# Kernel optimization log

Hardware: AMD Instinct MI355X
Metric: run time of the kernel (lower is better)

## Reference

```python
import jax, jax.numpy as jnp
import numpy as np

BATCH, SEQ, FEAT, UNITS, OUT = 128, 2048, 64, 64, 6


def setup_inputs() -> dict:
    key = jax.random.key(0)
    ks = jax.random.split(key, 12)
    s = 0.05
    inp = {
        "x": jax.random.normal(ks[0], (BATCH, SEQ, FEAT), dtype=jnp.float32),
        # LSTMCell 0 (kernel, recurrent_kernel, bias); gate order i,f,g,o
        "W0": jax.random.normal(ks[1], (FEAT, 4 * UNITS), dtype=jnp.float32) * s,
        "U0": jax.random.normal(ks[2], (UNITS, 4 * UNITS), dtype=jnp.float32) * s,
        "b0": jax.random.normal(ks[3], (4 * UNITS,), dtype=jnp.float32) * s,
        # LSTMCell 1 (shared by layers 2 AND 3, as in the original code)
        "W1": jax.random.normal(ks[4], (UNITS, 4 * UNITS), dtype=jnp.float32) * s,
        "U1": jax.random.normal(ks[5], (UNITS, 4 * UNITS), dtype=jnp.float32) * s,
        "b1": jax.random.normal(ks[6], (4 * UNITS,), dtype=jnp.float32) * s,
        # Dense heads
        "Wf": jax.random.normal(ks[7], (UNITS, 64), dtype=jnp.float32) * s,
        "bf": jax.random.normal(ks[8], (64,), dtype=jnp.float32) * s,
        "Wo": jax.random.normal(ks[9], (64, OUT), dtype=jnp.float32) * s,
        "bo": jax.random.normal(ks[10], (OUT,), dtype=jnp.float32) * s,
    }
    return inp


def _lstm_cell(c, h, xin, W, U, b):
    # Keras LSTMCell math, gate order i, f, g(candidate), o
    z = xin @ W + h @ U + b  # [B, 4U]
    i, f, g, o = jnp.split(z, 4, axis=-1)
    c_new = jax.nn.sigmoid(f) * c + jax.nn.sigmoid(i) * jnp.tanh(g)
    h_new = jax.nn.sigmoid(o) * jnp.tanh(c_new)
    return c_new, h_new


def reference(x, W0, U0, b0, W1, U1, b1, Wf, bf, Wo, bo):
    B = x.shape[0]
    z = jnp.zeros((B, UNITS), dtype=x.dtype)
    init = (z, z, z, z, z, z)  # (c0,h0,c1,h1,c2,h2)

    def step(carry, xt):
        c0, h0, c1, h1, c2, h2 = carry
        c0, h0 = _lstm_cell(c0, h0, xt, W0, U0, b0)
        c1, h1 = _lstm_cell(c1, h1, h0, W1, U1, b1)
        # NOTE: original code reuses rnn_cell1's weights for the 3rd layer
        c2, h2 = _lstm_cell(c2, h2, h1, W1, U1, b1)
        return (c0, h0, c1, h1, c2, h2), None

    xt = jnp.swapaxes(x, 0, 1)  # [T, B, F]
    (c0, h0, c1, h1, c2, h2), _ = jax.lax.scan(step, init, xt)
    y = jax.nn.relu(h2 @ Wf + bf)
    return y @ Wo + bo
```

## Files before the change

### kernel.cpp

```cpp
#include <hip/hip_runtime.h>

#define BATCHN 128
#define SEQT   2048
#define FEAT   64
#define UNITS  64
#define NCOL   256
#define OUTD   6
#define CH     20
#define BUF    96

typedef float v2f __attribute__((ext_vector_type(2)));

__device__ __forceinline__ float fast_exp2(float x) {
#if __has_builtin(__builtin_amdgcn_exp2f)
    return __builtin_amdgcn_exp2f(x);
#else
    return exp2f(x);
#endif
}
__device__ __forceinline__ float fast_rcp(float x) {
#if __has_builtin(__builtin_amdgcn_rcpf)
    return __builtin_amdgcn_rcpf(x);
#else
    return 1.0f / x;
#endif
}
__device__ __forceinline__ float sig_(float x) {
    return fast_rcp(1.0f + fast_exp2(-1.4426950408889634f * x));
}
__device__ __forceinline__ float tanh_(float x) {
    float xc = fminf(fmaxf(x, -15.0f), 15.0f);
    float e  = fast_exp2(2.8853900817779268f * xc);
    return (e - 1.0f) * fast_rcp(e + 1.0f);
}

__device__ __forceinline__ v2f pk_fma(v2f a, v2f b, v2f c) {
    return __builtin_elementwise_fma(a, b, c);
}

template<int CTRL>
__device__ __forceinline__ float dppf(float v) {
    return __builtin_bit_cast(float, __builtin_amdgcn_update_dpp(
        0, __builtin_bit_cast(int, v), CTRL, 0xF, 0xF, true));
}
__device__ __forceinline__ v2f red8v(v2f v) {
    v2f t;
    t.x = dppf<0xB1>(v.x);  t.y = dppf<0xB1>(v.y);  v = v + t;
    t.x = dppf<0x4E>(v.x);  t.y = dppf<0x4E>(v.y);  v = v + t;
    t.x = dppf<0x141>(v.x); t.y = dppf<0x141>(v.y); v = v + t;
    return v;
}

__global__ __launch_bounds__(768, 3)
void lstm3_g8(const float* __restrict__ x,
              const float* __restrict__ W0, const float* __restrict__ U0,
              const float* __restrict__ b0,
              const float* __restrict__ W1, const float* __restrict__ U1,
              const float* __restrict__ b1,
              const float* __restrict__ Wf, const float* __restrict__ bfv,
              const float* __restrict__ Wo, const float* __restrict__ bov,
              float* __restrict__ out)
{
    const int b   = blockIdx.x;
    const int tid = threadIdx.x;
    const int grp = tid >> 8;
    const int lt  = tid & 255;
    const int cg  = lt >> 3;
    const int kg  = lt & 7;
    const int up  = kg & 1;
    const int myu = 2 * cg + up;

    __shared__ __align__(16) float ls[8 * BUF];
    __shared__ float lact[UNITS];
    float* const lsb = ls;

    const float* Wsel = (grp == 0) ? W0 : W1;
    const float* Usel = (grp == 0) ? U0 : U1;
    const float* bsel = (grp == 0) ? b0 : b1;
    const float* Msel = (kg < 4) ? Wsel : Usel;

    v2f wt[16][4];
    float biasv[4];
#pragma unroll
    for (int g = 0; g < 4; ++g) {
        const int colb = (g << 6) + 2 * cg;
#pragma unroll
        for (int k = 0; k < 16; ++k) {
            const int r = (kg & 3) * 16 + k;
            wt[k][g] = (v2f){Msel[r * NCOL + colb], Msel[r * NCOL + colb + 1]};
        }
        biasv[g] = bsel[(g << 6) + myu];
    }

    if (tid < 6 * BUF) lsb[tid] = 0.f;

    const float* xbase = x + (size_t)b * SEQT * FEAT;
    const bool xload = (grp == 0) && (lt < 16);
    float* xwp0 = lsb + 6 * BUF + CH * (lt >> 2) + 4 * (lt & 3);
    float* xwp1 = xwp0 + BUF;
    if (xload) *(float4*)xwp1 = *(const float4*)(xbase + lt * 4);
    __syncthreads();

    const float* inB0 = (grp == 0) ? (lsb + 6 * BUF) : (lsb + (2 * (grp - 1) + 0) * BUF);
    const float* inB1 = inB0 + BUF;
    const float* rcB0 = lsb + (2 * grp + 0) * BUF;
    const float* rcB1 = rcB0 + BUF;
    const int chOff = (kg & 3) * CH;
    const float* opP0 = ((kg < 4) ? inB0 : rcB0) + chOff;
    const float* opP1 = ((kg < 4) ? inB1 : rcB1) + chOff;

    float* hwp0 = lsb + (2 * grp + 0) * BUF + CH * (myu >> 4) + (myu & 15);
    float* hwp1 = hwp0 + BUF;

    float c = 0.f;

    for (int tk = 0; tk < SEQT + 2; ++tk) {
        const int p = tk & 1;
        const int t = tk - grp;
        const bool active = (t >= 0) && (t < SEQT);

        float4 xg;
        const bool loading = xload && (tk + 1 < SEQT);
        if (loading)
            xg = *(const float4*)(xbase + (size_t)(tk + 1) * FEAT + lt * 4);

        if (active) {
            const float* op = p ? opP0 : opP1;
            float4 o0 = *(const float4*)(op);
            float4 o1 = *(const float4*)(op + 4);
            float4 o2 = *(const float4*)(op + 8);
            float4 o3 = *(const float4*)(op + 12);

            v2f acc[4];
#pragma unroll
            for (int g = 0; g < 4; ++g) acc[g] = (v2f){0.f, 0.f};

#define MAC(V, K)                                                     \
            {                                                         \
                v2f s = (v2f){(V), (V)};                              \
                acc[0] = pk_fma(s, wt[K][0], acc[0]);                 \
                acc[1] = pk_fma(s, wt[K][1], acc[1]);                 \
                acc[2] = pk_fma(s, wt[K][2], acc[2]);                 \
                acc[3] = pk_fma(s, wt[K][3], acc[3]);                 \
            }
            MAC(o0.x, 0)  MAC(o0.y, 1)  MAC(o0.z, 2)  MAC(o0.w, 3)
            MAC(o1.x, 4)  MAC(o1.y, 5)  MAC(o1.z, 6)  MAC(o1.w, 7)
            MAC(o2.x, 8)  MAC(o2.y, 9)  MAC(o2.z, 10) MAC(o2.w, 11)
            MAC(o3.x, 12) MAC(o3.y, 13) MAC(o3.z, 14) MAC(o3.w, 15)
#undef MAC

            v2f z0 = red8v(acc[0]);
            v2f z1 = red8v(acc[1]);
            v2f z2 = red8v(acc[2]);
            v2f z3 = red8v(acc[3]);

            const float zi = (up ? z0.y : z0.x) + biasv[0];
            const float zf = (up ? z1.y : z1.x) + biasv[1];
            const float zg = (up ? z2.y : z2.x) + biasv[2];
            const float zo = (up ? z3.y : z3.x) + biasv[3];

            const float ig = sig_(zi), fg = sig_(zf);
            const float gg = tanh_(zg), og = sig_(zo);
            c = fg * c + ig * gg;
            const float hn = og * tanh_(c);
            if (kg < 2) *(p ? hwp1 : hwp0) = hn;
        }

        if (loading)
            *(float4*)(p ? xwp1 : xwp0) = xg;

        __syncthreads();
    }

    const float* h2f = lsb + (2 * 2 + 1) * BUF;
    if (tid < UNITS) {
        float a = bfv[tid];
#pragma unroll
        for (int k = 0; k < UNITS; ++k)
            a += h2f[CH * (k >> 4) + (k & 15)] * Wf[k * 64 + tid];
        lact[tid] = fmaxf(a, 0.f);
    }
    __syncthreads();
    if (tid < OUTD) {
        float a = bov[tid];
#pragma unroll
        for (int k = 0; k < UNITS; ++k) a += lact[k] * Wo[k * OUTD + tid];
        out[b * OUTD + tid] = a;
    }
}

extern "C" void kernel_launch(void* const* d_in, const int* in_sizes, int n_in,
                              void* d_out, int out_size, void* d_ws, size_t ws_size,
                              hipStream_t stream) {
    const float* x   = (const float*)d_in[0];
    const float* W0  = (const float*)d_in[1];
    const float* U0  = (const float*)d_in[2];
    const float* b0  = (const float*)d_in[3];
    const float* W1  = (const float*)d_in[4];
    const float* U1  = (const float*)d_in[5];
    const float* b1  = (const float*)d_in[6];
    const float* Wf  = (const float*)d_in[7];
    const float* bfv = (const float*)d_in[8];
    const float* Wo  = (const float*)d_in[9];
    const float* bov = (const float*)d_in[10];
    float* out = (float*)d_out;

    lstm3_g8<<<BATCHN, 768, 0, stream>>>(x, W0, U0, b0, W1, U1, b1,
                                         Wf, bfv, Wo, bov, out);
}
```

Before: 2.006 ms.

## Prefetch x two steps ahead in registers, unroll by two, use raw barrier

The time loop is unrolled by two with fixed LDS buffer pointers per tick. The x input is prefetched two steps ahead into two register float4s and stored to LDS at the start of each tick, so global load latency is hidden across a whole step. The __syncthreads is replaced with an inline s_waitcnt lgkmcnt(0) plus s_barrier, which skips waiting on outstanding global loads, and the LDS chunk stride changes from 20 to 24. The risks are a bank-conflict shift from the new stride and correctness relying on vmcnt being handled implicitly before the LDS store.

```diff
diff --git a/kernel.cpp b/kernel.cpp
--- a/kernel.cpp
+++ b/kernel.cpp
@@ -6,7 +6,7 @@
 #define UNITS  64
 #define NCOL   256
 #define OUTD   6
-#define CH     20
+#define CH     24
 #define BUF    96
 
 typedef float v2f __attribute__((ext_vector_type(2)));
@@ -52,14 +52,14 @@
 }
 
 __global__ __launch_bounds__(768, 3)
-void lstm3_g8(const float* __restrict__ x,
-              const float* __restrict__ W0, const float* __restrict__ U0,
-              const float* __restrict__ b0,
-              const float* __restrict__ W1, const float* __restrict__ U1,
-              const float* __restrict__ b1,
-              const float* __restrict__ Wf, const float* __restrict__ bfv,
-              const float* __restrict__ Wo, const float* __restrict__ bov,
-              float* __restrict__ out)
+void lstm3_g8p(const float* __restrict__ x,
+               const float* __restrict__ W0, const float* __restrict__ U0,
+               const float* __restrict__ b0,
+               const float* __restrict__ W1, const float* __restrict__ U1,
+               const float* __restrict__ b1,
+               const float* __restrict__ Wf, const float* __restrict__ bfv,
+               const float* __restrict__ Wo, const float* __restrict__ bov,
+               float* __restrict__ out)
 {
     const int b   = blockIdx.x;
     const int tid = threadIdx.x;
@@ -98,79 +98,74 @@
     const bool xload = (grp == 0) && (lt < 16);
     float* xwp0 = lsb + 6 * BUF + CH * (lt >> 2) + 4 * (lt & 3);
     float* xwp1 = xwp0 + BUF;
-    if (xload) *(float4*)xwp1 = *(const float4*)(xbase + lt * 4);
+
+    float4 xr0, xr1;
+    if (xload) {
+        *(float4*)xwp1 = *(const float4*)(xbase + lt * 4);
+        xr0 = *(const float4*)(xbase + (size_t)1 * FEAT + lt * 4);
+        xr1 = *(const float4*)(xbase + (size_t)2 * FEAT + lt * 4);
+    }
     __syncthreads();
 
-    const float* inB0 = (grp == 0) ? (lsb + 6 * BUF) : (lsb + (2 * (grp - 1) + 0) * BUF);
+    const float* inB0 = (grp == 0) ? (lsb + 6 * BUF) : (lsb + (2 * (grp - 1)) * BUF);
     const float* inB1 = inB0 + BUF;
-    const float* rcB0 = lsb + (2 * grp + 0) * BUF;
+    const float* rcB0 = lsb + (2 * grp) * BUF;
     const float* rcB1 = rcB0 + BUF;
     const int chOff = (kg & 3) * CH;
     const float* opP0 = ((kg < 4) ? inB0 : rcB0) + chOff;
     const float* opP1 = ((kg < 4) ? inB1 : rcB1) + chOff;
 
-    float* hwp0 = lsb + (2 * grp + 0) * BUF + CH * (myu >> 4) + (myu & 15);
+    float* hwp0 = lsb + (2 * grp) * BUF + CH * (myu >> 4) + (myu & 15);
     float* hwp1 = hwp0 + BUF;
 
     float c = 0.f;
 
-    for (int tk = 0; tk < SEQT + 2; ++tk) {
-        const int p = tk & 1;
-        const int t = tk - grp;
-        const bool active = (t >= 0) && (t < SEQT);
-
-        float4 xg;
-        const bool loading = xload && (tk + 1 < SEQT);
-        if (loading)
-            xg = *(const float4*)(xbase + (size_t)(tk + 1) * FEAT + lt * 4);
-
-        if (active) {
-            const float* op = p ? opP0 : opP1;
-            float4 o0 = *(const float4*)(op);
-            float4 o1 = *(const float4*)(op + 4);
-            float4 o2 = *(const float4*)(op + 8);
-            float4 o3 = *(const float4*)(op + 12);
-
-            v2f acc[4];
-#pragma unroll
-            for (int g = 0; g < 4; ++g) acc[g] = (v2f){0.f, 0.f};
-
-#define MAC(V, K)                                                     \
-            {                                                         \
-                v2f s = (v2f){(V), (V)};                              \
-                acc[0] = pk_fma(s, wt[K][0], acc[0]);                 \
-                acc[1] = pk_fma(s, wt[K][1], acc[1]);                 \
-                acc[2] = pk_fma(s, wt[K][2], acc[2]);                 \
-                acc[3] = pk_fma(s, wt[K][3], acc[3]);                 \
-            }
-            MAC(o0.x, 0)  MAC(o0.y, 1)  MAC(o0.z, 2)  MAC(o0.w, 3)
-            MAC(o1.x, 4)  MAC(o1.y, 5)  MAC(o1.z, 6)  MAC(o1.w, 7)
-            MAC(o2.x, 8)  MAC(o2.y, 9)  MAC(o2.z, 10) MAC(o2.w, 11)
-            MAC(o3.x, 12) MAC(o3.y, 13) MAC(o3.z, 14) MAC(o3.w, 15)
-#undef MAC
-
-            v2f z0 = red8v(acc[0]);
-            v2f z1 = red8v(acc[1]);
-            v2f z2 = red8v(acc[2]);
-            v2f z3 = red8v(acc[3]);
-
-            const float zi = (up ? z0.y : z0.x) + biasv[0];
-            const float zf = (up ? z1.y : z1.x) + biasv[1];
-            const float zg = (up ? z2.y : z2.x) + biasv[2];
-            const float zo = (up ? z3.y : z3.x) + biasv[3];
-
-            const float ig = sig_(zi), fg = sig_(zf);
-            const float gg = tanh_(zg), og = sig_(zo);
-            c = fg * c + ig * gg;
-            const float hn = og * tanh_(c);
-            if (kg < 2) *(p ? hwp1 : hwp0) = hn;
-        }
-
-        if (loading)
-            *(float4*)(p ? xwp1 : xwp0) = xg;
-
-        __syncthreads();
-    }
+#define MAC1(V, K)                                                            \
+    { v2f s_; s_.x = (V); s_.y = (V);                                         \
+      a0 = pk_fma(s_, wt[K][0], a0);                                          \
+      a1 = pk_fma(s_, wt[K][1], a1);                                          \
+      a2 = pk_fma(s_, wt[K][2], a2);                                          \
+      a3 = pk_fma(s_, wt[K][3], a3); }
+
+#define TICK(TK, PUBW, XR)                                                    \
+    {                                                                         \
+        if (xload) {                                                          \
+            *(float4*)(PUBW) = (XR);                                          \
+            int tn = (TK) + 3; if (tn > SEQT - 1) tn = SEQT - 1;              \
+            (XR) = *(const float4*)(xbase + (size_t)tn * FEAT + lt * 4);      \
+        }                                                                     \
+        const int t_ = (TK) - grp;                                            \
+        if (t_ >= 0 && t_ < SEQT) {                                           \
+            const float* op = ((TK) & 1) ? opP0 : opP1;   \
+            float4 o0 = *(const float4*)(op);                                 \
+            float4 o1 = *(const float4*)(op + 4);                             \
+            float4 o2 = *(const float4*)(op + 8);                             \
+            float4 o3 = *(const float4*)(op + 12);                            \
+            v2f a0 = (v2f){0.f, 0.f}, a1 = a0, a2 = a0, a3 = a0;              \
+            MAC1(o0.x, 0)  MAC1(o0.y, 1)  MAC1(o0.z, 2)  MAC1(o0.w, 3)        \
+            MAC1(o1.x, 4)  MAC1(o1.y, 5)  MAC1(o1.z, 6)  MAC1(o1.w, 7)        \
+            MAC1(o2.x, 8)  MAC1(o2.y, 9)  MAC1(o2.z, 10) MAC1(o2.w, 11)       \
+            MAC1(o3.x, 12) MAC1(o3.y, 13) MAC1(o3.z, 14) MAC1(o3.w, 15)       \
+            v2f z0 = red8v(a0), z1 = red8v(a1), z2 = red8v(a2), z3 = red8v(a3);\
+            const float zi = (up ? z0.y : z0.x) + biasv[0];                   \
+            const float zf = (up ? z1.y : z1.x) + biasv[1];                   \
+            const float zg = (up ? z2.y : z2.x) + biasv[2];                   \
+            const float zo = (up ? z3.y : z3.x) + biasv[3];                   \
+            const float ig = sig_(zi), fg = sig_(zf);                         \
+            const float gg = tanh_(zg), og = sig_(zo);                        \
+            c = fg * c + ig * gg;                                             \
+            const float hn = og * tanh_(c);                                   \
+            if (kg < 2) *(((TK) & 1) ? hwp1 : hwp0) = hn;                     \
+        }                                                                     \
+        asm volatile("s_waitcnt lgkmcnt(0)\n\ts_barrier" ::: "memory");       \
+    }
+
+    for (int tk = 0; tk < SEQT + 2; tk += 2) {
+        TICK(tk,     xwp0, xr0)
+        TICK(tk + 1, xwp1, xr1)
+    }
+#undef TICK
+#undef MAC1
 
     const float* h2f = lsb + (2 * 2 + 1) * BUF;
     if (tid < UNITS) {
@@ -205,6 +200,6 @@
     const float* bov = (const float*)d_in[10];
     float* out = (float*)d_out;
 
-    lstm3_g8<<<BATCHN, 768, 0, stream>>>(x, W0, U0, b0, W1, U1, b1,
-                                         Wf, bfv, Wo, bov, out);
-}
+    lstm3_g8p<<<BATCHN, 768, 0, stream>>>(x, W0, U0, b0, W1, U1, b1,
+                                          Wf, bfv, Wo, bov, out);
+}
```

Result: slower. 2.235 ms (+11.4%).

## Prefetch x through an LDS ring with async global-to-LDS loads

Applied to the files above, without the earlier changes.

Input timesteps are now streamed with global_load_lds into an 8-slot LDS ring, six steps ahead, instead of a per-step register load followed by an LDS store in a double buffer. The block-wide __syncthreads is replaced by a hand-written s_waitcnt vmcnt(5) on the loading wave plus an lgkmcnt wait and s_barrier, so the barrier no longer waits for all outstanding global loads. The aim is to take global-memory latency off the serial per-step critical path of the recurrence. The chunk stride CH also changes from 20 to 24, which alters the LDS padding and bank mapping. The cost is reliance on inline asm wait counts matching the exact number of loads in flight, which is fragile if the compiler adds other vector-memory operations.

```diff
diff --git a/kernel.cpp b/kernel.cpp
--- a/kernel.cpp
+++ b/kernel.cpp
@@ -6,8 +6,10 @@
 #define UNITS  64
 #define NCOL   256
 #define OUTD   6
-#define CH     20
+#define CH     24
 #define BUF    96
+#define RING   8
+#define PFD    6
 
 typedef float v2f __attribute__((ext_vector_type(2)));
 
@@ -51,15 +53,21 @@
     return v;
 }
 
+__device__ __forceinline__ void gload16(float* lds, const float* g) {
+    __builtin_amdgcn_global_load_lds(
+        (const __attribute__((address_space(1))) void*)g,
+        (__attribute__((address_space(3))) void*)lds, 16, 0, 0);
+}
+
 __global__ __launch_bounds__(768, 3)
-void lstm3_g8(const float* __restrict__ x,
-              const float* __restrict__ W0, const float* __restrict__ U0,
-              const float* __restrict__ b0,
-              const float* __restrict__ W1, const float* __restrict__ U1,
-              const float* __restrict__ b1,
-              const float* __restrict__ Wf, const float* __restrict__ bfv,
-              const float* __restrict__ Wo, const float* __restrict__ bov,
-              float* __restrict__ out)
+void lstm3_ring(const float* __restrict__ x,
+                const float* __restrict__ W0, const float* __restrict__ U0,
+                const float* __restrict__ b0,
+                const float* __restrict__ W1, const float* __restrict__ U1,
+                const float* __restrict__ b1,
+                const float* __restrict__ Wf, const float* __restrict__ bfv,
+                const float* __restrict__ Wo, const float* __restrict__ bov,
+                float* __restrict__ out)
 {
     const int b   = blockIdx.x;
     const int tid = threadIdx.x;
@@ -70,7 +78,8 @@
     const int up  = kg & 1;
     const int myu = 2 * cg + up;
 
-    __shared__ __align__(16) float ls[8 * BUF];
+    __shared__ __align__(16) float ls[6 * BUF];
+    __shared__ __align__(16) float lxr[RING][FEAT];
     __shared__ float lact[UNITS];
     float* const lsb = ls;
 
@@ -95,65 +104,59 @@
     if (tid < 6 * BUF) lsb[tid] = 0.f;
 
     const float* xbase = x + (size_t)b * SEQT * FEAT;
-    const bool xload = (grp == 0) && (lt < 16);
-    float* xwp0 = lsb + 6 * BUF + CH * (lt >> 2) + 4 * (lt & 3);
-    float* xwp1 = xwp0 + BUF;
-    if (xload) *(float4*)xwp1 = *(const float4*)(xbase + lt * 4);
+    if (tid < 16) {
+#pragma unroll
+        for (int s = 0; s < PFD; ++s)
+            gload16(&lxr[s][0], xbase + (size_t)s * FEAT + tid * 4);
+    }
     __syncthreads();
 
-    const float* inB0 = (grp == 0) ? (lsb + 6 * BUF) : (lsb + (2 * (grp - 1) + 0) * BUF);
+    const float* inB0 = (grp == 0) ? lsb : (lsb + (2 * (grp - 1)) * BUF);
     const float* inB1 = inB0 + BUF;
-    const float* rcB0 = lsb + (2 * grp + 0) * BUF;
+    const float* rcB0 = lsb + (2 * grp) * BUF;
     const float* rcB1 = rcB0 + BUF;
     const int chOff = (kg & 3) * CH;
     const float* opP0 = ((kg < 4) ? inB0 : rcB0) + chOff;
     const float* opP1 = ((kg < 4) ? inB1 : rcB1) + chOff;
-
-    float* hwp0 = lsb + (2 * grp + 0) * BUF + CH * (myu >> 4) + (myu & 15);
+    const bool xlane = (grp == 0) && (kg < 4);
+
+    float* hwp0 = lsb + (2 * grp) * BUF + CH * (myu >> 4) + (myu & 15);
     float* hwp1 = hwp0 + BUF;
 
     float c = 0.f;
 
+#define MAC1(V, K)                                                            \
+    { v2f s_; s_.x = (V); s_.y = (V);                                         \
+      a0 = pk_fma(s_, wt[K][0], a0);                                          \
+      a1 = pk_fma(s_, wt[K][1], a1);                                          \
+      a2 = pk_fma(s_, wt[K][2], a2);                                          \
+      a3 = pk_fma(s_, wt[K][3], a3); }
+
     for (int tk = 0; tk < SEQT + 2; ++tk) {
-        const int p = tk & 1;
-        const int t = tk - grp;
-        const bool active = (t >= 0) && (t < SEQT);
-
-        float4 xg;
-        const bool loading = xload && (tk + 1 < SEQT);
-        if (loading)
-            xg = *(const float4*)(xbase + (size_t)(tk + 1) * FEAT + lt * 4);
-
-        if (active) {
-            const float* op = p ? opP0 : opP1;
+        if (tid < 16) {
+            const int tn = tk + PFD;
+            if (tn < SEQT)
+                gload16(&lxr[tn & (RING - 1)][0],
+                        xbase + (size_t)tn * FEAT + tid * 4);
+        }
+
+        const int t_ = tk - grp;
+        if (t_ >= 0 && t_ < SEQT) {
+            const float* op = (tk & 1) ? opP0 : opP1;
+            if (xlane) op = &lxr[tk & (RING - 1)][kg * 16];
+
             float4 o0 = *(const float4*)(op);
             float4 o1 = *(const float4*)(op + 4);
             float4 o2 = *(const float4*)(op + 8);
             float4 o3 = *(const float4*)(op + 12);
 
-            v2f acc[4];
-#pragma unroll
-            for (int g = 0; g < 4; ++g) acc[g] = (v2f){0.f, 0.f};
-
-#define MAC(V, K)                                                     \
-            {                                                         \
-                v2f s = (v2f){(V), (V)};                              \
-                acc[0] = pk_fma(s, wt[K][0], acc[0]);                 \
-                acc[1] = pk_fma(s, wt[K][1], acc[1]);                 \
-                acc[2] = pk_fma(s, wt[K][2], acc[2]);                 \
-                acc[3] = pk_fma(s, wt[K][3], acc[3]);                 \
-            }
-            MAC(o0.x, 0)  MAC(o0.y, 1)  MAC(o0.z, 2)  MAC(o0.w, 3)
-            MAC(o1.x, 4)  MAC(o1.y, 5)  MAC(o1.z, 6)  MAC(o1.w, 7)
-            MAC(o2.x, 8)  MAC(o2.y, 9)  MAC(o2.z, 10) MAC(o2.w, 11)
-            MAC(o3.x, 12) MAC(o3.y, 13) MAC(o3.z, 14) MAC(o3.w, 15)
-#undef MAC
-
-            v2f z0 = red8v(acc[0]);
-            v2f z1 = red8v(acc[1]);
-            v2f z2 = red8v(acc[2]);
-            v2f z3 = red8v(acc[3]);
-
+            v2f a0 = (v2f){0.f, 0.f}, a1 = a0, a2 = a0, a3 = a0;
+            MAC1(o0.x, 0)  MAC1(o0.y, 1)  MAC1(o0.z, 2)  MAC1(o0.w, 3)
+            MAC1(o1.x, 4)  MAC1(o1.y, 5)  MAC1(o1.z, 6)  MAC1(o1.w, 7)
+            MAC1(o2.x, 8)  MAC1(o2.y, 9)  MAC1(o2.z, 10) MAC1(o2.w, 11)
+            MAC1(o3.x, 12) MAC1(o3.y, 13) MAC1(o3.z, 14) MAC1(o3.w, 15)
+
+            v2f z0 = red8v(a0), z1 = red8v(a1), z2 = red8v(a2), z3 = red8v(a3);
             const float zi = (up ? z0.y : z0.x) + biasv[0];
             const float zf = (up ? z1.y : z1.x) + biasv[1];
             const float zg = (up ? z2.y : z2.x) + biasv[2];
@@ -163,14 +166,14 @@
             const float gg = tanh_(zg), og = sig_(zo);
             c = fg * c + ig * gg;
             const float hn = og * tanh_(c);
-            if (kg < 2) *(p ? hwp1 : hwp0) = hn;
+            if (kg < 2) *((tk & 1) ? hwp1 : hwp0) = hn;
         }
 
-        if (loading)
-            *(float4*)(p ? xwp1 : xwp0) = xg;
-
-        __syncthreads();
-    }
+        if ((tid >> 6) == 0)
+            asm volatile("s_waitcnt vmcnt(5)" ::: "memory");
+        asm volatile("s_waitcnt lgkmcnt(0)\n\ts_barrier" ::: "memory");
+    }
+#undef MAC1
 
     const float* h2f = lsb + (2 * 2 + 1) * BUF;
     if (tid < UNITS) {
@@ -205,6 +208,6 @@
     const float* bov = (const float*)d_in[10];
     float* out = (float*)d_out;
 
-    lstm3_g8<<<BATCHN, 768, 0, stream>>>(x, W0, U0, b0, W1, U1, b1,
-                                         Wf, bfv, Wo, bov, out);
-}
+    lstm3_ring<<<BATCHN, 768, 0, stream>>>(x, W0, U0, b0, W1, U1, b1,
+                                           Wf, bfv, Wo, bov, out);
+}
```

After: 2.138 ms. +6.6%, slower.
